# Kernel optimization log

Hardware: AMD Instinct MI355X
Metric: run time of the kernel (lower is better)

## Reference

```python
import jax, jax.numpy as jnp
import numpy as np

DIM = 192
HEADS = 4
EPS = 1e-12  # F.normalize default eps


def setup_inputs() -> dict:
    key = jax.random.key(0)
    k0, k1, k2, k3 = jax.random.split(key, 4)
    x = jax.random.normal(k0, (4, DIM, 128, 128), dtype=jnp.float32)
    # qkv 1x1 conv weight: [3*dim, dim, 1, 1] -> stored as [3*dim, dim]
    w_qkv = jax.random.normal(k1, (3 * DIM, DIM), dtype=jnp.float32) * (1.0 / np.sqrt(DIM))
    # depthwise 3x3 conv weight: [3*dim, 1, 3, 3]
    w_dw = jax.random.normal(k2, (3 * DIM, 1, 3, 3), dtype=jnp.float32) * (1.0 / 3.0)
    # project_out 1x1 conv weight: [dim, dim]
    w_proj = jax.random.normal(k3, (DIM, DIM), dtype=jnp.float32) * (1.0 / np.sqrt(DIM))
    # temperature: ones(heads,1,1), requires_grad=False in original
    temperature = jnp.ones((HEADS, 1, 1), dtype=jnp.float32)
    return {"x": x, "w_qkv": w_qkv, "w_dw": w_dw, "w_proj": w_proj,
            "temperature": temperature}


def _l2norm(t):
    # F.normalize(t, dim=-1): t / max(||t||_2, eps)
    n = jnp.sqrt(jnp.sum(t * t, axis=-1, keepdims=True))
    return t / jnp.maximum(n, EPS)


def reference(x, w_qkv, w_dw, w_proj, temperature):
    b, c, h, w = x.shape
    ch = c // HEADS  # channels per head
    # 1x1 conv (no bias) == channel GEMM
    qkv = jnp.einsum('oc,bchw->bohw', w_qkv, x)
    # depthwise 3x3 conv, padding=1, groups=3*dim
    qkv = jax.lax.conv_general_dilated(
        qkv, w_dw, window_strides=(1, 1), padding=((1, 1), (1, 1)),
        dimension_numbers=('NCHW', 'OIHW', 'NCHW'),
        feature_group_count=3 * c)
    q, k, v = jnp.split(qkv, 3, axis=1)
    # b (head ch) h w -> b head ch (h w)
    def rearr(t):
        return t.reshape(b, HEADS, ch, h * w)
    q, k, v = rearr(q), rearr(k), rearr(v)
    q = _l2norm(q)
    k = _l2norm(k)
    # channel-channel attention: [b, head, ch, ch]
    attn = jnp.einsum('bhcn,bhdn->bhcd', q, k) * temperature[None]
    attn = jax.nn.softmax(attn, axis=-1)
    out = jnp.einsum('bhcd,bhdn->bhcn', attn, v)
    out = out.reshape(b, c, h, w)
    out = jnp.einsum('oc,bchw->bohw', w_proj, out)
    return out
```

## Files before the change

kernel.cpp:

```cpp
#include <hip/hip_runtime.h>

typedef unsigned short u16;
typedef float f32x4 __attribute__((ext_vector_type(4)));
typedef __bf16 bf16x8 __attribute__((ext_vector_type(8)));
typedef unsigned short u16x8 __attribute__((ext_vector_type(8)));
typedef unsigned short u16x4 __attribute__((ext_vector_type(4)));

#define DEV static __device__ __forceinline__

DEV u16 f2bf(float f) {
  unsigned int u = __float_as_uint(f);
  u += 0x7FFFu + ((u >> 16) & 1u);
  return (u16)(u >> 16);
}
DEV float bf2f(u16 h) { return __uint_as_float(((unsigned int)h) << 16); }

DEV void gload_lds16(const void* g, void* l) {
  __builtin_amdgcn_global_load_lds(
      (__attribute__((address_space(1))) void*)(unsigned long long)g,
      (__attribute__((address_space(3))) void*)l, 16, 0, 0);
}

__global__ __launch_bounds__(256) void convert_w_kernel(
    const float* __restrict__ in, u16* __restrict__ out, int n) {
  int i = blockIdx.x * 256 + threadIdx.x;
  if (i < n) out[i] = f2bf(in[i]);
}

template <bool IN_F32, bool OUT_BF16, int NJ>
__global__ __launch_bounds__(256, 2) void gemm_bt_kernel(
    const void* __restrict__ Av, const u16* __restrict__ B,
    void* __restrict__ Cv, size_t aBatch, size_t bBatch, size_t cBatch,
    int ldC) {
  __shared__ __align__(16) char smem[73728];
  char* sA = smem;
  char* sB = smem + 49152;

  const int tid = threadIdx.x, wave = tid >> 6, lane = tid & 63;
  const int id = blockIdx.x;
  const int m0 = (id & 127) * 128, b = id >> 7;

  if (IN_F32) {
    const float* Xb = (const float*)Av + (size_t)b * aBatch + m0;
    const int cbl = tid & 7, iq = tid >> 3;
#pragma unroll
    for (int pass = 0; pass < 6; ++pass) {
      const int cb = pass * 8 + cbl;
      f32x4 v[4];
#pragma unroll
      for (int r = 0; r < 4; ++r)
        v[r] = *(const f32x4*)(Xb + (size_t)(cb * 4 + r) * 16384 + iq * 4);
#pragma unroll
      for (int j = 0; j < 4; ++j) {
        const int n = iq * 4 + j;
        u16x4 col;
        col[0] = f2bf(v[0][j]);
        col[1] = f2bf(v[1][j]);
        col[2] = f2bf(v[2][j]);
        col[3] = f2bf(v[3][j]);
        *(u16x4*)(sA + n * 384 + ((cb * 8) ^ ((n & 7) << 4))) = col;
      }
    }
  } else {
    const u16* Vb = (const u16*)Av + (size_t)b * aBatch + m0;
    const int cbl = tid & 15, iq = tid >> 4;
#pragma unroll
    for (int pass = 0; pass < 3; ++pass) {
      const int cb = pass * 16 + cbl;
      u16x8 v[4];
#pragma unroll
      for (int r = 0; r < 4; ++r)
        v[r] = *(const u16x8*)(Vb + (size_t)(cb * 4 + r) * 16384 + iq * 8);
#pragma unroll
      for (int j = 0; j < 8; ++j) {
        const int n = iq * 8 + j;
        u16x4 col;
        col[0] = v[0][j];
        col[1] = v[1][j];
        col[2] = v[2][j];
        col[3] = v[3][j];
        *(u16x4*)(sA + n * 384 + ((cb * 8) ^ ((n & 7) << 4))) = col;
      }
    }
  }
  const char* Bbase = (const char*)(B + (size_t)b * bBatch);
#pragma unroll
  for (int i = 0; i < 6; ++i) {
    const int c = i * 4 + wave;
    const int d = c * 1024 + lane * 16;
    const int row = d / 384, inrow = d - row * 384;
    gload_lds16(Bbase + row * 384 + (inrow ^ ((row & 7) << 4)), sB + c * 1024);
  }
  asm volatile("s_waitcnt vmcnt(0) lgkmcnt(0)" ::: "memory");
  __builtin_amdgcn_s_barrier();

  const int wm = wave & 1, wn = wave >> 1;
  const int l15 = lane & 15, lg = lane >> 4;
  const int swm = (l15 & 7) << 4;
  const int rA0 = (wm * 64 + l15) * 384;
  const int rB0 = (wn * 32 + l15) * 384;

  bf16x8 af[4][6];
#pragma unroll
  for (int mi = 0; mi < 4; ++mi)
#pragma unroll
    for (int ks = 0; ks < 6; ++ks)
      af[mi][ks] = *(const bf16x8*)(sA + rA0 + mi * 16 * 384 +
                                    ((ks * 64 + lg * 16) ^ swm));

  f32x4 acc[4][2];
  for (int j = 0; j < NJ; ++j) {
    if (j > 0) {
      const int j0 = (j - 1) * 64;
      if (OUT_BF16) {
        u16* Cb = (u16*)Cv + (size_t)b * cBatch;
#pragma unroll
        for (int mi = 0; mi < 4; ++mi)
#pragma unroll
          for (int nj = 0; nj < 2; ++nj) {
            u16x4 ov;
#pragma unroll
            for (int r = 0; r < 4; ++r) ov[r] = f2bf(acc[mi][nj][r]);
            *(u16x4*)(Cb + (size_t)(j0 + wn * 32 + nj * 16 + l15) * ldC + m0 +
                      wm * 64 + mi * 16 + lg * 4) = ov;
          }
      } else {
        float* Cb = (float*)Cv + (size_t)b * cBatch;
#pragma unroll
        for (int mi = 0; mi < 4; ++mi)
#pragma unroll
          for (int nj = 0; nj < 2; ++nj)
            *(f32x4*)(Cb + (size_t)(j0 + wn * 32 + nj * 16 + l15) * ldC + m0 +
                      wm * 64 + mi * 16 + lg * 4) = acc[mi][nj];
      }
    }
    bf16x8 bfv[2][6];
#pragma unroll
    for (int nj = 0; nj < 2; ++nj)
#pragma unroll
      for (int ks = 0; ks < 6; ++ks)
        bfv[nj][ks] = *(const bf16x8*)(sB + rB0 + nj * 16 * 384 +
                                       ((ks * 64 + lg * 16) ^ swm));
    asm volatile("s_waitcnt lgkmcnt(0)" ::: "memory");
    __builtin_amdgcn_s_barrier();
    if (j + 1 < NJ) {
      const char* Bj = Bbase + (size_t)(j + 1) * 64 * 384;
#pragma unroll
      for (int i = 0; i < 6; ++i) {
        const int c = i * 4 + wave;
        const int d = c * 1024 + lane * 16;
        const int row = d / 384, inrow = d - row * 384;
        gload_lds16(Bj + row * 384 + (inrow ^ ((row & 7) << 4)), sB + c * 1024);
      }
    }
    __builtin_amdgcn_sched_barrier(0);
#pragma unroll
    for (int mi = 0; mi < 4; ++mi)
#pragma unroll
      for (int nj = 0; nj < 2; ++nj) acc[mi][nj] = (f32x4){0.f, 0.f, 0.f, 0.f};
#pragma unroll
    for (int ks = 0; ks < 6; ++ks)
#pragma unroll
      for (int mi = 0; mi < 4; ++mi)
#pragma unroll
        for (int nj = 0; nj < 2; ++nj)
          acc[mi][nj] = __builtin_amdgcn_mfma_f32_16x16x32_bf16(
              af[mi][ks], bfv[nj][ks], acc[mi][nj], 0, 0, 0);
    if (j + 1 < NJ) {
      asm volatile("s_waitcnt vmcnt(0)" ::: "memory");
      __builtin_amdgcn_s_barrier();
    }
  }
  {
    const int j0 = (NJ - 1) * 64;
    if (OUT_BF16) {
      u16* Cb = (u16*)Cv + (size_t)b * cBatch;
#pragma unroll
      for (int mi = 0; mi < 4; ++mi)
#pragma unroll
        for (int nj = 0; nj < 2; ++nj) {
          u16x4 ov;
#pragma unroll
          for (int r = 0; r < 4; ++r) ov[r] = f2bf(acc[mi][nj][r]);
          *(u16x4*)(Cb + (size_t)(j0 + wn * 32 + nj * 16 + l15) * ldC + m0 +
                    wm * 64 + mi * 16 + lg * 4) = ov;
        }
    } else {
      float* Cb = (float*)Cv + (size_t)b * cBatch;
#pragma unroll
      for (int mi = 0; mi < 4; ++mi)
#pragma unroll
        for (int nj = 0; nj < 2; ++nj)
          *(f32x4*)(Cb + (size_t)(j0 + wn * 32 + nj * 16 + l15) * ldC + m0 +
                    wm * 64 + mi * 16 + lg * 4) = acc[mi][nj];
    }
  }
}

__global__ __launch_bounds__(256) void dwconv_kernel(
    u16* __restrict__ qkv, const float* __restrict__ wdw,
    float* __restrict__ sq) {
  __shared__ u16 img[16384];
  __shared__ float red[4];
  const int o = blockIdx.x, b = blockIdx.y;
  const size_t base = ((size_t)b * 576 + o) * 16384;
  const int tid = threadIdx.x, wave = tid >> 6, lane = tid & 63;
#pragma unroll
  for (int i = 0; i < 8; ++i) {
    const int off = (i * 4 + wave) * 1024;
    gload_lds16((const char*)qkv + base * 2 + off + lane * 16, (char*)img + off);
  }
  asm volatile("s_waitcnt vmcnt(0)" ::: "memory");
  __syncthreads();
  float w[9];
#pragma unroll
  for (int j = 0; j < 9; ++j) w[j] = wdw[o * 9 + j];
  float sqacc = 0.f;
  for (int it = 0; it < 8; ++it) {
    const int chunk = it * 256 + tid;
    const int px0 = chunk * 8;
    const int y = px0 >> 7, x0 = px0 & 127;
    float acc[8];
#pragma unroll
    for (int j = 0; j < 8; ++j) acc[j] = 0.f;
#pragma unroll
    for (int dy = -1; dy <= 1; ++dy) {
      const int yy = y + dy;
      float v[10];
      if (yy >= 0 && yy <= 127) {
        const u16* rowp = img + yy * 128 + x0;
        u16x8 m = *(const u16x8*)rowp;
#pragma unroll
        for (int j = 0; j < 8; ++j) v[j + 1] = bf2f(m[j]);
        v[0] = (x0 > 0) ? bf2f(rowp[-1]) : 0.f;
        v[9] = (x0 < 120) ? bf2f(rowp[8]) : 0.f;
      } else {
#pragma unroll
        for (int j = 0; j < 10; ++j) v[j] = 0.f;
      }
      const float w0 = w[(dy + 1) * 3], w1 = w[(dy + 1) * 3 + 1],
                  w2 = w[(dy + 1) * 3 + 2];
#pragma unroll
      for (int j = 0; j < 8; ++j) acc[j] += w0 * v[j] + w1 * v[j + 1] + w2 * v[j + 2];
    }
    u16x8 ov;
#pragma unroll
    for (int j = 0; j < 8; ++j) {
      sqacc += acc[j] * acc[j];
      ov[j] = f2bf(acc[j]);
    }
    *(u16x8*)(qkv + base + px0) = ov;
  }
#pragma unroll
  for (int s = 32; s > 0; s >>= 1) sqacc += __shfl_xor(sqacc, s, 64);
  if (lane == 0) red[wave] = sqacc;
  __syncthreads();
  if (tid == 0) sq[b * 576 + o] = red[0] + red[1] + red[2] + red[3];
}

__global__ __launch_bounds__(256) void gram_kernel(
    const u16* __restrict__ qkv, float* __restrict__ partial) {
  __shared__ u16 tiles[4 * 3072];
  __shared__ float red[4 * 2304];
  const int bh = blockIdx.y, b = bh >> 2, h = bh & 3;
  const int g = blockIdx.x;
  const int wave = threadIdx.x >> 6, lane = threadIdx.x & 63;
  const int n0 = g * 512 + wave * 128;
  const u16* qb = qkv + ((size_t)b * 576 + h * 48) * 16384;
  const u16* kb = qb + (size_t)192 * 16384;
  char* tl = (char*)(tiles + wave * 3072);
  const int l15 = lane & 15, lg = lane >> 4;
  const int swz = (l15 & 3) << 4;
  f32x4 acc[3][3];
#pragma unroll
  for (int i = 0; i < 3; ++i)
#pragma unroll
    for (int j = 0; j < 3; ++j) acc[i][j] = (f32x4){0.f, 0.f, 0.f, 0.f};

  for (int ks = 0; ks < 4; ++ks) {
    const int nn = n0 + ks * 32;
    asm volatile("s_waitcnt lgkmcnt(0)" ::: "memory");
#pragma unroll
    for (int i = 0; i < 6; ++i) {
      const int flat = i * 1024 + lane * 16;
      const int row = flat >> 6, colb = flat & 63;
      const u16* src = (row < 48) ? (qb + (size_t)row * 16384 + nn)
                                  : (kb + (size_t)(row - 48) * 16384 + nn);
      gload_lds16((const char*)src + (colb ^ ((row & 3) << 4)), tl + i * 1024);
    }
    asm volatile("s_waitcnt vmcnt(0)" ::: "memory");
    bf16x8 qf[3], kf[3];
#pragma unroll
    for (int f = 0; f < 3; ++f) {
      qf[f] = *(const bf16x8*)(tl + (f * 16 + l15) * 64 + ((lg * 16) ^ swz));
      kf[f] = *(const bf16x8*)(tl + (48 + f * 16 + l15) * 64 + ((lg * 16) ^ swz));
    }
#pragma unroll
    for (int i = 0; i < 3; ++i)
#pragma unroll
      for (int j = 0; j < 3; ++j)
        acc[i][j] = __builtin_amdgcn_mfma_f32_16x16x32_bf16(qf[i], kf[j],
                                                            acc[i][j], 0, 0, 0);
  }
  {
    float* rw = red + wave * 2304;
#pragma unroll
    for (int i = 0; i < 3; ++i)
#pragma unroll
      for (int j = 0; j < 3; ++j)
#pragma unroll
        for (int r = 0; r < 4; ++r)
          rw[(i * 16 + lg * 4 + r) * 48 + (j * 16 + l15)] = acc[i][j][r];
  }
  __syncthreads();
#pragma unroll
  for (int it = 0; it < 9; ++it) {
    const int p = it * 256 + threadIdx.x;
    const float s = red[p] + red[2304 + p] + red[4608 + p] + red[6912 + p];
    partial[((size_t)bh * 2304 + p) * 32 + g] = s;
  }
}

__global__ __launch_bounds__(256) void softmax_weff_kernel(
    const float* __restrict__ partial, const float* __restrict__ sq,
    const float* __restrict__ temp, const float* __restrict__ wproj,
    u16* __restrict__ weff) {
  __shared__ float G[2304];
  __shared__ float wp[192 * 49];
  __shared__ float nq[48], nk[48];
  const int bh = blockIdx.x, b = bh >> 2, h = bh & 3;
  const int tid = threadIdx.x;
#pragma unroll
  for (int it = 0; it < 36; ++it) {
    const int j = it * 256 + tid;
    const int o = j / 48, c = j - o * 48;
    wp[o * 49 + c] = wproj[o * 192 + h * 48 + c];
  }
#pragma unroll
  for (int it = 0; it < 9; ++it) {
    const int p = it * 256 + tid;
    const f32x4* pp = (const f32x4*)(partial + ((size_t)bh * 2304 + p) * 32);
    const f32x4 a = (pp[0] + pp[1]) + (pp[2] + pp[3]) +
                    (pp[4] + pp[5]) + (pp[6] + pp[7]);
    G[p] = a.x + a.y + a.z + a.w;
  }
  if (tid < 48) {
    nq[tid] = fmaxf(sqrtf(sq[b * 576 + h * 48 + tid]), 1e-12f);
    nk[tid] = fmaxf(sqrtf(sq[b * 576 + 192 + h * 48 + tid]), 1e-12f);
  }
  __syncthreads();
  if (tid < 48) {
    const int r = tid;
    const float inq = temp[h] / nq[r];
    float L[48];
    float mx = -3.4e38f;
#pragma unroll 4
    for (int d = 0; d < 48; ++d) {
      const float v = G[r * 48 + d] * inq / nk[d];
      L[d] = v;
      mx = fmaxf(mx, v);
    }
    float s = 0.f;
#pragma unroll 4
    for (int d = 0; d < 48; ++d) {
      const float e = __expf(L[d] - mx);
      L[d] = e;
      s += e;
    }
    const float inv = 1.f / s;
#pragma unroll 4
    for (int d = 0; d < 48; ++d) G[r * 48 + d] = L[d] * inv;
  }
  __syncthreads();
  if (tid < 192) {
    const int o = tid;
    f32x4 acc[12];
#pragma unroll
    for (int dv = 0; dv < 12; ++dv) acc[dv] = (f32x4){0.f, 0.f, 0.f, 0.f};
    for (int c = 0; c < 48; ++c) {
      const float w = wp[o * 49 + c];
      const f32x4* at = (const f32x4*)(G + c * 48);
#pragma unroll
      for (int dv = 0; dv < 12; ++dv) acc[dv] += w * at[dv];
    }
    u16* op = weff + ((size_t)b * 192 + o) * 192 + h * 48;
#pragma unroll
    for (int g8 = 0; g8 < 6; ++g8) {
      u16x8 ov;
#pragma unroll
      for (int j = 0; j < 8; ++j) {
        const int d = g8 * 8 + j;
        ov[j] = f2bf(acc[d >> 2][d & 3]);
      }
      *(u16x8*)(op + g8 * 8) = ov;
    }
  }
}

extern "C" void kernel_launch(void* const* d_in, const int* in_sizes, int n_in,
                              void* d_out, int out_size, void* d_ws,
                              size_t ws_size, hipStream_t stream) {
  (void)in_sizes; (void)n_in; (void)out_size; (void)ws_size;
  const float* x      = (const float*)d_in[0];
  const float* w_qkv  = (const float*)d_in[1];
  const float* w_dw   = (const float*)d_in[2];
  const float* w_proj = (const float*)d_in[3];
  const float* temp   = (const float*)d_in[4];

  char* ws = (char*)d_ws;
  u16*   qkv     = (u16*)ws;
  float* partial = (float*)(ws + 75497472);
  float* sq      = (float*)(ws + 80216064);
  u16*   Wq      = (u16*)(ws + 80225280);
  u16*   Weff    = (u16*)(ws + 80446464);

  convert_w_kernel<<<dim3(432), 256, 0, stream>>>(w_qkv, Wq, 110592);
  gemm_bt_kernel<true, true, 9><<<dim3(512), 256, 0, stream>>>(
      x, Wq, qkv, (size_t)192 * 16384, 0, (size_t)576 * 16384, 16384);
  dwconv_kernel<<<dim3(576, 4), 256, 0, stream>>>(qkv, w_dw, sq);
  gram_kernel<<<dim3(32, 16), 256, 0, stream>>>(qkv, partial);
  softmax_weff_kernel<<<dim3(16), 256, 0, stream>>>(partial, sq, temp, w_proj,
                                                    Weff);
  gemm_bt_kernel<false, false, 3><<<dim3(512), 256, 0, stream>>>(
      qkv + (size_t)384 * 16384, Weff, d_out, (size_t)576 * 16384,
      (size_t)192 * 192, (size_t)192 * 16384, 16384);
}
```

Before: 137.3 us.

## Halve GEMM M-tile, raise occupancy, overlap stores, and split partial-sum reduction

```diff
diff --git a/kernel.cpp b/kernel.cpp
--- a/kernel.cpp
+++ b/kernel.cpp
@@ -28,24 +28,24 @@
 }
 
 template <bool IN_F32, bool OUT_BF16, int NJ>
-__global__ __launch_bounds__(256, 2) void gemm_bt_kernel(
+__global__ __launch_bounds__(256, 3) void gemm_bt_kernel(
     const void* __restrict__ Av, const u16* __restrict__ B,
     void* __restrict__ Cv, size_t aBatch, size_t bBatch, size_t cBatch,
     int ldC) {
-  __shared__ __align__(16) char smem[73728];
+  __shared__ __align__(16) char smem[49152];
   char* sA = smem;
-  char* sB = smem + 49152;
+  char* sB = smem + 24576;
 
   const int tid = threadIdx.x, wave = tid >> 6, lane = tid & 63;
   const int id = blockIdx.x;
-  const int m0 = (id & 127) * 128, b = id >> 7;
+  const int m0 = (id & 255) * 64, b = id >> 8;
 
   if (IN_F32) {
     const float* Xb = (const float*)Av + (size_t)b * aBatch + m0;
-    const int cbl = tid & 7, iq = tid >> 3;
-#pragma unroll
-    for (int pass = 0; pass < 6; ++pass) {
-      const int cb = pass * 8 + cbl;
+    const int cbl = tid & 15, iq = tid >> 4;
+#pragma unroll
+    for (int pass = 0; pass < 3; ++pass) {
+      const int cb = pass * 16 + cbl;
       f32x4 v[4];
 #pragma unroll
       for (int r = 0; r < 4; ++r)
@@ -63,23 +63,25 @@
     }
   } else {
     const u16* Vb = (const u16*)Av + (size_t)b * aBatch + m0;
-    const int cbl = tid & 15, iq = tid >> 4;
-#pragma unroll
-    for (int pass = 0; pass < 3; ++pass) {
-      const int cb = pass * 16 + cbl;
-      u16x8 v[4];
-#pragma unroll
-      for (int r = 0; r < 4; ++r)
-        v[r] = *(const u16x8*)(Vb + (size_t)(cb * 4 + r) * 16384 + iq * 8);
-#pragma unroll
-      for (int j = 0; j < 8; ++j) {
-        const int n = iq * 8 + j;
-        u16x4 col;
-        col[0] = v[0][j];
-        col[1] = v[1][j];
-        col[2] = v[2][j];
-        col[3] = v[3][j];
-        *(u16x4*)(sA + n * 384 + ((cb * 8) ^ ((n & 7) << 4))) = col;
+#pragma unroll
+    for (int pass = 0; pass < 2; ++pass) {
+      const int task = pass * 256 + tid;
+      if (task < 384) {
+        const int cb = task >> 3, io = task & 7;
+        u16x8 v[4];
+#pragma unroll
+        for (int r = 0; r < 4; ++r)
+          v[r] = *(const u16x8*)(Vb + (size_t)(cb * 4 + r) * 16384 + io * 8);
+#pragma unroll
+        for (int j = 0; j < 8; ++j) {
+          const int n = io * 8 + j;
+          u16x4 col;
+          col[0] = v[0][j];
+          col[1] = v[1][j];
+          col[2] = v[2][j];
+          col[3] = v[3][j];
+          *(u16x4*)(sA + n * 384 + ((cb * 8) ^ ((n & 7) << 4))) = col;
+        }
       }
     }
   }
@@ -97,43 +99,20 @@
   const int wm = wave & 1, wn = wave >> 1;
   const int l15 = lane & 15, lg = lane >> 4;
   const int swm = (l15 & 7) << 4;
-  const int rA0 = (wm * 64 + l15) * 384;
+  const int rA0 = (wm * 32 + l15) * 384;
   const int rB0 = (wn * 32 + l15) * 384;
 
-  bf16x8 af[4][6];
-#pragma unroll
-  for (int mi = 0; mi < 4; ++mi)
+  bf16x8 af[2][6];
+#pragma unroll
+  for (int mi = 0; mi < 2; ++mi)
 #pragma unroll
     for (int ks = 0; ks < 6; ++ks)
       af[mi][ks] = *(const bf16x8*)(sA + rA0 + mi * 16 * 384 +
                                     ((ks * 64 + lg * 16) ^ swm));
 
-  f32x4 acc[4][2];
+  f32x4 acc[2][2];
+#pragma unroll 1
   for (int j = 0; j < NJ; ++j) {
-    if (j > 0) {
-      const int j0 = (j - 1) * 64;
-      if (OUT_BF16) {
-        u16* Cb = (u16*)Cv + (size_t)b * cBatch;
-#pragma unroll
-        for (int mi = 0; mi < 4; ++mi)
-#pragma unroll
-          for (int nj = 0; nj < 2; ++nj) {
-            u16x4 ov;
-#pragma unroll
-            for (int r = 0; r < 4; ++r) ov[r] = f2bf(acc[mi][nj][r]);
-            *(u16x4*)(Cb + (size_t)(j0 + wn * 32 + nj * 16 + l15) * ldC + m0 +
-                      wm * 64 + mi * 16 + lg * 4) = ov;
-          }
-      } else {
-        float* Cb = (float*)Cv + (size_t)b * cBatch;
-#pragma unroll
-        for (int mi = 0; mi < 4; ++mi)
-#pragma unroll
-          for (int nj = 0; nj < 2; ++nj)
-            *(f32x4*)(Cb + (size_t)(j0 + wn * 32 + nj * 16 + l15) * ldC + m0 +
-                      wm * 64 + mi * 16 + lg * 4) = acc[mi][nj];
-      }
-    }
     bf16x8 bfv[2][6];
 #pragma unroll
     for (int nj = 0; nj < 2; ++nj)
@@ -144,7 +123,7 @@
     asm volatile("s_waitcnt lgkmcnt(0)" ::: "memory");
     __builtin_amdgcn_s_barrier();
     if (j + 1 < NJ) {
-      const char* Bj = Bbase + (size_t)(j + 1) * 64 * 384;
+      const char* Bj = Bbase + (size_t)(j + 1) * 24576;
 #pragma unroll
       for (int i = 0; i < 6; ++i) {
         const int c = i * 4 + wave;
@@ -153,21 +132,48 @@
         gload_lds16(Bj + row * 384 + (inrow ^ ((row & 7) << 4)), sB + c * 1024);
       }
     }
+    if (j > 0) {
+      const int j0 = (j - 1) * 64;
+      if (OUT_BF16) {
+        u16* Cb = (u16*)Cv + (size_t)b * cBatch;
+#pragma unroll
+        for (int mi = 0; mi < 2; ++mi)
+#pragma unroll
+          for (int nj = 0; nj < 2; ++nj) {
+            u16x4 ov;
+#pragma unroll
+            for (int r = 0; r < 4; ++r) ov[r] = f2bf(acc[mi][nj][r]);
+            *(u16x4*)(Cb + (size_t)(j0 + wn * 32 + nj * 16 + l15) * ldC + m0 +
+                      wm * 32 + mi * 16 + lg * 4) = ov;
+          }
+      } else {
+        float* Cb = (float*)Cv + (size_t)b * cBatch;
+#pragma unroll
+        for (int mi = 0; mi < 2; ++mi)
+#pragma unroll
+          for (int nj = 0; nj < 2; ++nj)
+            *(f32x4*)(Cb + (size_t)(j0 + wn * 32 + nj * 16 + l15) * ldC + m0 +
+                      wm * 32 + mi * 16 + lg * 4) = acc[mi][nj];
+      }
+    }
     __builtin_amdgcn_sched_barrier(0);
 #pragma unroll
-    for (int mi = 0; mi < 4; ++mi)
+    for (int mi = 0; mi < 2; ++mi)
 #pragma unroll
       for (int nj = 0; nj < 2; ++nj) acc[mi][nj] = (f32x4){0.f, 0.f, 0.f, 0.f};
 #pragma unroll
     for (int ks = 0; ks < 6; ++ks)
 #pragma unroll
-      for (int mi = 0; mi < 4; ++mi)
+      for (int mi = 0; mi < 2; ++mi)
 #pragma unroll
         for (int nj = 0; nj < 2; ++nj)
           acc[mi][nj] = __builtin_amdgcn_mfma_f32_16x16x32_bf16(
               af[mi][ks], bfv[nj][ks], acc[mi][nj], 0, 0, 0);
     if (j + 1 < NJ) {
-      asm volatile("s_waitcnt vmcnt(0)" ::: "memory");
+      if (j == 0)
+        asm volatile("s_waitcnt vmcnt(0)" ::: "memory");
+      else
+        asm volatile("s_waitcnt vmcnt(4)" ::: "memory");
       __builtin_amdgcn_s_barrier();
     }
   }
@@ -176,23 +182,23 @@
     if (OUT_BF16) {
       u16* Cb = (u16*)Cv + (size_t)b * cBatch;
 #pragma unroll
-      for (int mi = 0; mi < 4; ++mi)
+      for (int mi = 0; mi < 2; ++mi)
 #pragma unroll
         for (int nj = 0; nj < 2; ++nj) {
           u16x4 ov;
 #pragma unroll
           for (int r = 0; r < 4; ++r) ov[r] = f2bf(acc[mi][nj][r]);
           *(u16x4*)(Cb + (size_t)(j0 + wn * 32 + nj * 16 + l15) * ldC + m0 +
-                    wm * 64 + mi * 16 + lg * 4) = ov;
+                    wm * 32 + mi * 16 + lg * 4) = ov;
         }
     } else {
       float* Cb = (float*)Cv + (size_t)b * cBatch;
 #pragma unroll
-      for (int mi = 0; mi < 4; ++mi)
+      for (int mi = 0; mi < 2; ++mi)
 #pragma unroll
         for (int nj = 0; nj < 2; ++nj)
           *(f32x4*)(Cb + (size_t)(j0 + wn * 32 + nj * 16 + l15) * ldC + m0 +
-                    wm * 64 + mi * 16 + lg * 4) = acc[mi][nj];
+                    wm * 32 + mi * 16 + lg * 4) = acc[mi][nj];
     }
   }
 }
@@ -321,8 +327,17 @@
   }
 }
 
+__global__ __launch_bounds__(256) void reduce_partial_kernel(
+    const float* __restrict__ partial, float* __restrict__ G) {
+  const int idx = blockIdx.x * 256 + threadIdx.x;
+  const f32x4* pp = (const f32x4*)(partial + (size_t)idx * 32);
+  const f32x4 a = (pp[0] + pp[1]) + (pp[2] + pp[3]) +
+                  (pp[4] + pp[5]) + (pp[6] + pp[7]);
+  G[idx] = a.x + a.y + a.z + a.w;
+}
+
 __global__ __launch_bounds__(256) void softmax_weff_kernel(
-    const float* __restrict__ partial, const float* __restrict__ sq,
+    const float* __restrict__ Gin, const float* __restrict__ sq,
     const float* __restrict__ temp, const float* __restrict__ wproj,
     u16* __restrict__ weff) {
   __shared__ float G[2304];
@@ -339,10 +354,7 @@
 #pragma unroll
   for (int it = 0; it < 9; ++it) {
     const int p = it * 256 + tid;
-    const f32x4* pp = (const f32x4*)(partial + ((size_t)bh * 2304 + p) * 32);
-    const f32x4 a = (pp[0] + pp[1]) + (pp[2] + pp[3]) +
-                    (pp[4] + pp[5]) + (pp[6] + pp[7]);
-    G[p] = a.x + a.y + a.z + a.w;
+    G[p] = Gin[(size_t)bh * 2304 + p];
   }
   if (tid < 48) {
     nq[tid] = fmaxf(sqrtf(sq[b * 576 + h * 48 + tid]), 1e-12f);
@@ -410,18 +422,19 @@
   char* ws = (char*)d_ws;
   u16*   qkv     = (u16*)ws;
   float* partial = (float*)(ws + 75497472);
-  float* sq      = (float*)(ws + 80216064);
-  u16*   Wq      = (u16*)(ws + 80225280);
-  u16*   Weff    = (u16*)(ws + 80446464);
+  float* G       = (float*)(ws + 80216064);
+  float* sq      = (float*)(ws + 80363520);
+  u16*   Wq      = (u16*)(ws + 80372736);
+  u16*   Weff    = (u16*)(ws + 80593920);
 
   convert_w_kernel<<<dim3(432), 256, 0, stream>>>(w_qkv, Wq, 110592);
-  gemm_bt_kernel<true, true, 9><<<dim3(512), 256, 0, stream>>>(
+  gemm_bt_kernel<true, true, 9><<<dim3(1024), 256, 0, stream>>>(
       x, Wq, qkv, (size_t)192 * 16384, 0, (size_t)576 * 16384, 16384);
   dwconv_kernel<<<dim3(576, 4), 256, 0, stream>>>(qkv, w_dw, sq);
   gram_kernel<<<dim3(32, 16), 256, 0, stream>>>(qkv, partial);
-  softmax_weff_kernel<<<dim3(16), 256, 0, stream>>>(partial, sq, temp, w_proj,
-                                                    Weff);
-  gemm_bt_kernel<false, false, 3><<<dim3(512), 256, 0, stream>>>(
+  reduce_partial_kernel<<<dim3(144), 256, 0, stream>>>(partial, G);
+  softmax_weff_kernel<<<dim3(16), 256, 0, stream>>>(G, sq, temp, w_proj, Weff);
+  gemm_bt_kernel<false, false, 3><<<dim3(1024), 256, 0, stream>>>(
       qkv + (size_t)384 * 16384, Weff, d_out, (size_t)576 * 16384,
       (size_t)192 * 192, (size_t)192 * 16384, 16384);
 }
```

After: 131.7 us. 4.0% less time.
